# Performance work log

Measured on AMD Instinct MI355X. Metric: run time of the kernel, lower is better.

Reference implementation:

```python
import jax, jax.numpy as jnp
import numpy as np

NUM_CLASSES = 1000
FEAT = 192
HID = 256
TOTAL_NODES = 8192  # 16 images * 512 patches, kNN is global (no batch vector in source)


def _knn_idx(x, k):
    # squared euclidean distances, top-k smallest (self-loop included: d(i,i)=0)
    sq = jnp.sum(x * x, axis=-1)                       # [N]
    d = sq[:, None] + sq[None, :] - 2.0 * (x @ x.T)    # [N, N]
    _, idx = jax.lax.top_k(-d, k)                      # [N, k] neighbor indices per node
    return idx


def _sage_conv(x, idx, w_l, b_l, w_r):
    # PyG SAGEConv (mean aggr): lin_l(mean_j x_j) + lin_r(x_i); bias on lin_l
    agg = jnp.mean(x[idx], axis=1)                     # [N, C_in] mean over k neighbors
    return agg @ w_l + b_l + x @ w_r


def setup_inputs() -> dict:
    key = jax.random.key(0)
    ks = jax.random.split(key, 8)
    s = lambda fi, fo: (2.0 / (fi + fo)) ** 0.5
    return {
        "x": jax.random.normal(ks[0], (TOTAL_NODES, FEAT), dtype=jnp.float32),
        "w_l0": jax.random.normal(ks[1], (FEAT, HID), jnp.float32) * s(FEAT, HID),
        "b_l0": jnp.zeros((HID,), jnp.float32),
        "w_r0": jax.random.normal(ks[2], (FEAT, HID), jnp.float32) * s(FEAT, HID),
        "w_l1": jax.random.normal(ks[3], (HID, HID), jnp.float32) * s(HID, HID),
        "b_l1": jnp.zeros((HID,), jnp.float32),
        "w_r1": jax.random.normal(ks[4], (HID, HID), jnp.float32) * s(HID, HID),
        "w_l2": jax.random.normal(ks[5], (HID, NUM_CLASSES), jnp.float32) * s(HID, NUM_CLASSES),
        "b_l2": jnp.zeros((NUM_CLASSES,), jnp.float32),
        "w_r2": jax.random.normal(ks[6], (HID, NUM_CLASSES), jnp.float32) * s(HID, NUM_CLASSES),
        "k": 9,
        "batch_size": 16,
    }


def reference(x, w_l0, b_l0, w_r0, w_l1, b_l1, w_r1, w_l2, b_l2, w_r2, k, batch_size):
    idx = _knn_idx(x, k)  # graph built once from input features, reused by all layers
    h = jax.nn.relu(_sage_conv(x, idx, w_l0, b_l0, w_r0))
    h = jax.nn.relu(_sage_conv(h, idx, w_l1, b_l1, w_r1))
    h = jax.nn.relu(_sage_conv(h, idx, w_l2, b_l2, w_r2))
    # global_mean_pool with batch = arange(B).repeat_interleave(N/B): equal-size segments
    h = h.reshape(batch_size, -1, h.shape[-1]).mean(axis=1)  # [B, num_classes]
    return h
```

## Files before the change

kernel.cpp:

```cpp
#include <hip/hip_runtime.h>

#define NN   8192
#define FEAT 192
#define HID  256
#define NCLS 1000
#define KNN  9
#define NPP  512
#define NIMG 16
#define KD   192
#define KL0  384

typedef unsigned short ushort_t;
typedef unsigned int uint_t;
typedef __attribute__((ext_vector_type(8))) __bf16 bf16x8;
typedef __attribute__((ext_vector_type(4))) float f32x4;

#define ASYNC16(gptr, lptr)                                                  \
  __builtin_amdgcn_global_load_lds(                                          \
      (const __attribute__((address_space(1))) void*)(gptr),                 \
      (__attribute__((address_space(3))) void*)(lptr), 16, 0, 0)

__device__ __forceinline__ ushort_t f2bf_rne(float f) {
  unsigned u = __float_as_uint(f);
  u += 0x7FFF + ((u >> 16) & 1);
  return (ushort_t)(u >> 16);
}
__device__ __forceinline__ float bf2f(ushort_t u) {
  return __uint_as_float((unsigned)u << 16);
}

__device__ __forceinline__ uint_t packkey(float f, int col) {
  uint_t b = __float_as_uint(f);
  uint_t m = (uint_t)((int)b >> 31) | 0x80000000u;
  uint_t u = b ^ m;
  return (u & 0xFFFFE000u) | (uint_t)col;
}

__device__ __forceinline__ void bubble9(uint_t (&tk)[KNN], uint_t k) {
#pragma unroll
  for (int p = 0; p < KNN; ++p) {
    uint_t lo = min(tk[p], k);
    k = max(tk[p], k);
    tk[p] = lo;
  }
}

__global__ __launch_bounds__(256) void k_norms_split(
    const float* __restrict__ x, float* __restrict__ sq,
    ushort_t* __restrict__ xs) {
  int wid  = (blockIdx.x * 256 + threadIdx.x) >> 6;
  int lane = threadIdx.x & 63;
  if (wid >= NN) return;
  const float* row = x + (size_t)wid * FEAT;
  ushort_t* xr = xs + (size_t)wid * KD;
  float s = 0.f;
#pragma unroll
  for (int f0 = 0; f0 < FEAT; f0 += 64) {
    int f = f0 + lane;
    float v = row[f];
    s += v * v;
    xr[f] = f2bf_rne(v);
  }
#pragma unroll
  for (int off = 32; off > 0; off >>= 1) s += __shfl_down(s, off);
  if (lane == 0) sq[wid] = s;
}

__global__ __launch_bounds__(256, 4) void k_dist_topk(
    const ushort_t* __restrict__ xs, const float* __restrict__ sq,
    uint_t* __restrict__ cand) {
  __shared__ __align__(16) char smem[24576];
  ushort_t* As = (ushort_t*)smem;
  ushort_t* Bs = (ushort_t*)(smem + 8192);
  uint_t*   Ms = (uint_t*)(smem + 19456);

  const int t    = threadIdx.x;
  const int lane = t & 63;
  const int w    = t >> 6;
  const int l15  = lane & 15, lq = lane >> 4;
  const int rowStart = blockIdx.y * 128;
  const int colStart = blockIdx.x * 128;
  const int mrow = (w >> 1) * 64;
  const int ncol = (w & 1) * 64;

  const int m0 = w * 128 + lane;
  const int r0 = m0 >> 2, r1 = r0 + 16;
  const int g0 = m0 & 3;
  const int gs0 = g0 ^ (r0 & 3);
  const int gs1 = g0 ^ (r1 & 3);
  const ushort_t* gA0 = xs + (size_t)(rowStart + r0) * KD + gs0 * 8;
  const ushort_t* gA1 = xs + (size_t)(rowStart + r1) * KD + gs1 * 8;
  const ushort_t* gB0 = xs + (size_t)(colStart + r0) * KD + gs0 * 8;
  const ushort_t* gB1 = xs + (size_t)(colStart + r1) * KD + gs1 * 8;
  ushort_t* lA = As + w * 1024;
  ushort_t* lB = Bs + w * 1024;

  const int pg = (lq ^ (l15 & 3)) * 8;
  int aoff[4], boff[4];
#pragma unroll
  for (int ti = 0; ti < 4; ++ti) aoff[ti] = (mrow + ti * 16 + l15) * 32 + pg;
#pragma unroll
  for (int tj = 0; tj < 4; ++tj) boff[tj] = (ncol + tj * 16 + l15) * 32 + pg;

  f32x4 c00 = {}, c01 = {}, c02 = {}, c03 = {};
  f32x4 c10 = {}, c11 = {}, c12 = {}, c13 = {};
  f32x4 c20 = {}, c21 = {}, c22 = {}, c23 = {};
  f32x4 c30 = {}, c31 = {}, c32 = {}, c33 = {};

#pragma unroll 1
  for (int kt = 0; kt < 6; ++kt) {
    const int k0 = kt * 32;
    ASYNC16(gA0 + k0, lA);
    ASYNC16(gA1 + k0, lA + 512);
    ASYNC16(gB0 + k0, lB);
    ASYNC16(gB1 + k0, lB + 512);
    __syncthreads();
    bf16x8 a0 = *(const bf16x8*)(As + aoff[0]);
    bf16x8 a1 = *(const bf16x8*)(As + aoff[1]);
    bf16x8 a2 = *(const bf16x8*)(As + aoff[2]);
    bf16x8 a3 = *(const bf16x8*)(As + aoff[3]);
    bf16x8 b0 = *(const bf16x8*)(Bs + boff[0]);
    bf16x8 b1 = *(const bf16x8*)(Bs + boff[1]);
    bf16x8 b2 = *(const bf16x8*)(Bs + boff[2]);
    bf16x8 b3 = *(const bf16x8*)(Bs + boff[3]);
    c00 = __builtin_amdgcn_mfma_f32_16x16x32_bf16(a0, b0, c00, 0, 0, 0);
    c01 = __builtin_amdgcn_mfma_f32_16x16x32_bf16(a0, b1, c01, 0, 0, 0);
    c02 = __builtin_amdgcn_mfma_f32_16x16x32_bf16(a0, b2, c02, 0, 0, 0);
    c03 = __builtin_amdgcn_mfma_f32_16x16x32_bf16(a0, b3, c03, 0, 0, 0);
    c10 = __builtin_amdgcn_mfma_f32_16x16x32_bf16(a1, b0, c10, 0, 0, 0);
    c11 = __builtin_amdgcn_mfma_f32_16x16x32_bf16(a1, b1, c11, 0, 0, 0);
    c12 = __builtin_amdgcn_mfma_f32_16x16x32_bf16(a1, b2, c12, 0, 0, 0);
    c13 = __builtin_amdgcn_mfma_f32_16x16x32_bf16(a1, b3, c13, 0, 0, 0);
    c20 = __builtin_amdgcn_mfma_f32_16x16x32_bf16(a2, b0, c20, 0, 0, 0);
    c21 = __builtin_amdgcn_mfma_f32_16x16x32_bf16(a2, b1, c21, 0, 0, 0);
    c22 = __builtin_amdgcn_mfma_f32_16x16x32_bf16(a2, b2, c22, 0, 0, 0);
    c23 = __builtin_amdgcn_mfma_f32_16x16x32_bf16(a2, b3, c23, 0, 0, 0);
    c30 = __builtin_amdgcn_mfma_f32_16x16x32_bf16(a3, b0, c30, 0, 0, 0);
    c31 = __builtin_amdgcn_mfma_f32_16x16x32_bf16(a3, b1, c31, 0, 0, 0);
    c32 = __builtin_amdgcn_mfma_f32_16x16x32_bf16(a3, b2, c32, 0, 0, 0);
    c33 = __builtin_amdgcn_mfma_f32_16x16x32_bf16(a3, b3, c33, 0, 0, 0);
    __syncthreads();
  }

  uint_t tk[KNN];
#pragma unroll
  for (int n = 0; n < KNN; ++n) tk[n] = 0xFFFFFFFFu;

  uint_t* Ew = (uint_t*)smem + w * (64 * 19);

#define EPI_ROW(TI, CV)                                                      \
  do {                                                                       \
    f32x4 v_ = (CV);                                                         \
    Ew[((TI) * 16 + lq * 4 + 0) * 19 + l15] =                                \
        packkey(fmaf(-2.0f, v_.x, sqv), mycol);                              \
    Ew[((TI) * 16 + lq * 4 + 1) * 19 + l15] =                                \
        packkey(fmaf(-2.0f, v_.y, sqv), mycol);                              \
    Ew[((TI) * 16 + lq * 4 + 2) * 19 + l15] =                                \
        packkey(fmaf(-2.0f, v_.z, sqv), mycol);                              \
    Ew[((TI) * 16 + lq * 4 + 3) * 19 + l15] =                                \
        packkey(fmaf(-2.0f, v_.w, sqv), mycol);                              \
  } while (0)

#define EPI_TILE(TJ, C0, C1, C2, C3)                                         \
  do {                                                                       \
    int mycol = colStart + ncol + (TJ) * 16 + l15;                           \
    float sqv = sq[mycol];                                                   \
    EPI_ROW(0, C0); EPI_ROW(1, C1); EPI_ROW(2, C2); EPI_ROW(3, C3);          \
    _Pragma("unroll")                                                        \
    for (int c = 0; c < 16; ++c) bubble9(tk, Ew[lane * 19 + c]);             \
  } while (0)

  EPI_TILE(0, c00, c10, c20, c30);
  EPI_TILE(1, c01, c11, c21, c31);
  EPI_TILE(2, c02, c12, c22, c32);
  EPI_TILE(3, c03, c13, c23, c33);

  __syncthreads();
  if (w & 1) {
#pragma unroll
    for (int n = 0; n < KNN; ++n) Ms[(mrow + lane) * 10 + n] = tk[n];
  }
  __syncthreads();
  if (!(w & 1)) {
#pragma unroll
    for (int n = 0; n < KNN; ++n) bubble9(tk, Ms[(mrow + lane) * 10 + n]);
    size_t base = (((size_t)(rowStart + mrow + lane)) * 64 + blockIdx.x) * KNN;
#pragma unroll
    for (int n = 0; n < KNN; ++n) cand[base + n] = tk[n];
  }
}

__global__ __launch_bounds__(256) void k_reduce_gather(
    const uint_t* __restrict__ cand, const float* __restrict__ x,
    int* __restrict__ idx, ushort_t* __restrict__ Ab0) {
  int wid  = (blockIdx.x * 256 + threadIdx.x) >> 6;
  int lane = threadIdx.x & 63;
  if (wid >= NN) return;
  const uint_t* cv = cand + (size_t)wid * 576;
  uint_t tk[KNN];
#pragma unroll
  for (int n = 0; n < KNN; ++n) tk[n] = 0xFFFFFFFFu;
#pragma unroll
  for (int m = 0; m < KNN; ++m) bubble9(tk, cv[lane + 64 * m]);

  int nb[KNN];
  for (int r = 0; r < KNN; ++r) {
    uint_t bm = tk[0];
#pragma unroll
    for (int off = 32; off > 0; off >>= 1)
      bm = min(bm, (uint_t)__shfl_xor((unsigned int)bm, off));
    if (tk[0] == bm) {
#pragma unroll
      for (int p = 0; p < KNN - 1; ++p) tk[p] = tk[p + 1];
      tk[KNN - 1] = 0xFFFFFFFFu;
    }
    nb[r] = (int)(bm & 0x1FFFu);
    if (lane == 0) idx[wid * KNN + r] = nb[r];
  }

#pragma unroll
  for (int f0 = 0; f0 < FEAT; f0 += 64) {
    int f = f0 + lane;
    float s = 0.f;
#pragma unroll
    for (int n = 0; n < KNN; ++n) s += x[(size_t)nb[n] * FEAT + f];
    Ab0[(size_t)wid * KL0 + f]        = f2bf_rne(s * (1.0f / KNN));
    Ab0[(size_t)wid * KL0 + FEAT + f] = f2bf_rne(x[(size_t)wid * FEAT + f]);
  }
}

__global__ __launch_bounds__(256) void k_cast_w(
    const float* __restrict__ w_l0, const float* __restrict__ w_r0,
    const float* __restrict__ w_l1, const float* __restrict__ w_r1,
    const float* __restrict__ w_l2, const float* __restrict__ w_r2,
    ushort_t* __restrict__ WT0, ushort_t* __restrict__ WT1,
    ushort_t* __restrict__ WT2, float* __restrict__ out) {
  int i = blockIdx.x * 256 + threadIdx.x;
  if (i < NIMG * NCLS) out[i] = 0.f;
  if (i < 98304) {
    int n = i / 384, k = i - n * 384;
    float v = (k < 192) ? w_l0[k * 256 + n] : w_r0[(k - 192) * 256 + n];
    WT0[i] = f2bf_rne(v);
  } else if (i < 98304 + 131072) {
    int j = i - 98304;
    int n = j / 512, k = j - n * 512;
    float v = (k < 256) ? w_l1[k * 256 + n] : w_r1[(k - 256) * 256 + n];
    WT1[j] = f2bf_rne(v);
  } else {
    int j = i - (98304 + 131072);
    int n = j / 512, k = j - n * 512;
    float v = 0.f;
    if (n < NCLS)
      v = (k < 256) ? w_l2[k * NCLS + n] : w_r2[(k - 256) * NCLS + n];
    WT2[j] = f2bf_rne(v);
  }
}

__global__ __launch_bounds__(256) void k_gather_h(
    const ushort_t* __restrict__ hsrc, const int* __restrict__ idx,
    ushort_t* __restrict__ adst) {
  int wid  = (blockIdx.x * 256 + threadIdx.x) >> 6;
  int lane = threadIdx.x & 63;
  if (wid >= NN) return;
  int nb[KNN];
#pragma unroll
  for (int n = 0; n < KNN; ++n) nb[n] = idx[wid * KNN + n];
  const int c0 = lane * 4;
  float s0 = 0.f, s1 = 0.f, s2 = 0.f, s3 = 0.f;
#pragma unroll
  for (int n = 0; n < KNN; ++n) {
    ushort4 v = *(const ushort4*)(hsrc + (size_t)nb[n] * 512 + c0);
    s0 += bf2f(v.x); s1 += bf2f(v.y); s2 += bf2f(v.z); s3 += bf2f(v.w);
  }
  ushort4 o;
  o.x = f2bf_rne(s0 * (1.0f / KNN));
  o.y = f2bf_rne(s1 * (1.0f / KNN));
  o.z = f2bf_rne(s2 * (1.0f / KNN));
  o.w = f2bf_rne(s3 * (1.0f / KNN));
  *(ushort4*)(adst + (size_t)wid * 512 + c0) = o;
}

__global__ __launch_bounds__(256, 4) void k_sage64(
    const ushort_t* __restrict__ Ab, const ushort_t* __restrict__ WT,
    const float* __restrict__ bias, ushort_t* __restrict__ hdst, int KT) {
  __shared__ __align__(16) char smem[12288];
  ushort_t* As = (ushort_t*)smem;
  ushort_t* Bs = (ushort_t*)(smem + 8192);

  const int t    = threadIdx.x;
  const int lane = t & 63;
  const int w    = t >> 6;
  const int l15  = lane & 15, lq = lane >> 4;
  const int rowStart = blockIdx.y * 128;
  const int colStart = blockIdx.x * 64;
  const int mrow = (w >> 1) * 64;
  const int ncol = (w & 1) * 32;

  const int rA0 = t >> 2, rA1 = rA0 + 64;
  const int g   = t & 3;
  const int gsA0 = g ^ (rA0 & 3), gsA1 = g ^ (rA1 & 3);
  const ushort_t* gA0 = Ab + (size_t)(rowStart + rA0) * KT + gsA0 * 8;
  const ushort_t* gA1 = Ab + (size_t)(rowStart + rA1) * KT + gsA1 * 8;
  const ushort_t* gB0 = WT + (size_t)(colStart + rA0) * KT + gsA0 * 8;
  ushort_t* lA0 = As + w * 512;
  ushort_t* lA1 = As + 2048 + w * 512;
  ushort_t* lB0 = Bs + w * 512;

  const int pg = (lq ^ (l15 & 3)) * 8;
  int aoff[4], boff[2];
#pragma unroll
  for (int ti = 0; ti < 4; ++ti) aoff[ti] = (mrow + ti * 16 + l15) * 32 + pg;
#pragma unroll
  for (int tj = 0; tj < 2; ++tj) boff[tj] = (ncol + tj * 16 + l15) * 32 + pg;

  f32x4 c00 = {}, c01 = {};
  f32x4 c10 = {}, c11 = {};
  f32x4 c20 = {}, c21 = {};
  f32x4 c30 = {}, c31 = {};

  const int nkt = KT >> 5;
#pragma unroll 1
  for (int kt = 0; kt < nkt; ++kt) {
    const int k0 = kt * 32;
    ASYNC16(gA0 + k0, lA0);
    ASYNC16(gA1 + k0, lA1);
    ASYNC16(gB0 + k0, lB0);
    __syncthreads();
    bf16x8 a0 = *(const bf16x8*)(As + aoff[0]);
    bf16x8 a1 = *(const bf16x8*)(As + aoff[1]);
    bf16x8 a2 = *(const bf16x8*)(As + aoff[2]);
    bf16x8 a3 = *(const bf16x8*)(As + aoff[3]);
    bf16x8 b0 = *(const bf16x8*)(Bs + boff[0]);
    bf16x8 b1 = *(const bf16x8*)(Bs + boff[1]);
    c00 = __builtin_amdgcn_mfma_f32_16x16x32_bf16(a0, b0, c00, 0, 0, 0);
    c01 = __builtin_amdgcn_mfma_f32_16x16x32_bf16(a0, b1, c01, 0, 0, 0);
    c10 = __builtin_amdgcn_mfma_f32_16x16x32_bf16(a1, b0, c10, 0, 0, 0);
    c11 = __builtin_amdgcn_mfma_f32_16x16x32_bf16(a1, b1, c11, 0, 0, 0);
    c20 = __builtin_amdgcn_mfma_f32_16x16x32_bf16(a2, b0, c20, 0, 0, 0);
    c21 = __builtin_amdgcn_mfma_f32_16x16x32_bf16(a2, b1, c21, 0, 0, 0);
    c30 = __builtin_amdgcn_mfma_f32_16x16x32_bf16(a3, b0, c30, 0, 0, 0);
    c31 = __builtin_amdgcn_mfma_f32_16x16x32_bf16(a3, b1, c31, 0, 0, 0);
    __syncthreads();
  }

  const float bv0 = bias[colStart + ncol + l15];
  const float bv1 = bias[colStart + ncol + 16 + l15];

#define S64_STORE(TI, TJ, CV, BV)                                            \
  do {                                                                       \
    f32x4 v_ = (CV);                                                         \
    int col_ = colStart + ncol + (TJ) * 16 + l15;                            \
    size_t rb_ = (size_t)(rowStart + mrow + (TI) * 16 + lq * 4);             \
    hdst[(rb_ + 0) * 512 + col_] = f2bf_rne(fmaxf(v_.x + (BV), 0.f));        \
    hdst[(rb_ + 1) * 512 + col_] = f2bf_rne(fmaxf(v_.y + (BV), 0.f));        \
    hdst[(rb_ + 2) * 512 + col_] = f2bf_rne(fmaxf(v_.z + (BV), 0.f));        \
    hdst[(rb_ + 3) * 512 + col_] = f2bf_rne(fmaxf(v_.w + (BV), 0.f));        \
  } while (0)

  S64_STORE(0, 0, c00, bv0); S64_STORE(0, 1, c01, bv1);
  S64_STORE(1, 0, c10, bv0); S64_STORE(1, 1, c11, bv1);
  S64_STORE(2, 0, c20, bv0); S64_STORE(2, 1, c21, bv1);
  S64_STORE(3, 0, c30, bv0); S64_STORE(3, 1, c31, bv1);
}

__global__ __launch_bounds__(256, 2) void k_sage128_pool(
    const ushort_t* __restrict__ Ab, const ushort_t* __restrict__ WT,
    const float* __restrict__ bias, float* __restrict__ out) {
  __shared__ __align__(16) char smem[16384];
  ushort_t* As = (ushort_t*)smem;
  ushort_t* Bs = (ushort_t*)(smem + 8192);
  __shared__ float Ps[2][128];

  const int t    = threadIdx.x;
  const int lane = t & 63;
  const int w    = t >> 6;
  const int l15  = lane & 15, lq = lane >> 4;
  const int rowStart = blockIdx.y * 128;
  const int colStart = blockIdx.x * 128;
  const int mrow = (w >> 1) * 64;
  const int ncol = (w & 1) * 64;
  const int KT = 512;

  const int rA0 = t >> 2, rA1 = rA0 + 64;
  const int g   = t & 3;
  const int gsA0 = g ^ (rA0 & 3), gsA1 = g ^ (rA1 & 3);
  const ushort_t* gA0 = Ab + (size_t)(rowStart + rA0) * KT + gsA0 * 8;
  const ushort_t* gA1 = Ab + (size_t)(rowStart + rA1) * KT + gsA1 * 8;
  const ushort_t* gB0 = WT + (size_t)(colStart + rA0) * KT + gsA0 * 8;
  const ushort_t* gB1 = WT + (size_t)(colStart + rA1) * KT + gsA1 * 8;
  ushort_t* lA0 = As + w * 512;
  ushort_t* lA1 = As + 2048 + w * 512;
  ushort_t* lB0 = Bs + w * 512;
  ushort_t* lB1 = Bs + 2048 + w * 512;

  const int pg = (lq ^ (l15 & 3)) * 8;
  int aoff[4], boff[4];
#pragma unroll
  for (int ti = 0; ti < 4; ++ti) aoff[ti] = (mrow + ti * 16 + l15) * 32 + pg;
#pragma unroll
  for (int tj = 0; tj < 4; ++tj) boff[tj] = (ncol + tj * 16 + l15) * 32 + pg;

  f32x4 c00 = {}, c01 = {}, c02 = {}, c03 = {};
  f32x4 c10 = {}, c11 = {}, c12 = {}, c13 = {};
  f32x4 c20 = {}, c21 = {}, c22 = {}, c23 = {};
  f32x4 c30 = {}, c31 = {}, c32 = {}, c33 = {};

#pragma unroll 1
  for (int kt = 0; kt < 16; ++kt) {
    const int k0 = kt * 32;
    ASYNC16(gA0 + k0, lA0);
    ASYNC16(gA1 + k0, lA1);
    ASYNC16(gB0 + k0, lB0);
    ASYNC16(gB1 + k0, lB1);
    __syncthreads();
    bf16x8 a0 = *(const bf16x8*)(As + aoff[0]);
    bf16x8 a1 = *(const bf16x8*)(As + aoff[1]);
    bf16x8 a2 = *(const bf16x8*)(As + aoff[2]);
    bf16x8 a3 = *(const bf16x8*)(As + aoff[3]);
    bf16x8 b0 = *(const bf16x8*)(Bs + boff[0]);
    bf16x8 b1 = *(const bf16x8*)(Bs + boff[1]);
    bf16x8 b2 = *(const bf16x8*)(Bs + boff[2]);
    bf16x8 b3 = *(const bf16x8*)(Bs + boff[3]);
    c00 = __builtin_amdgcn_mfma_f32_16x16x32_bf16(a0, b0, c00, 0, 0, 0);
    c01 = __builtin_amdgcn_mfma_f32_16x16x32_bf16(a0, b1, c01, 0, 0, 0);
    c02 = __builtin_amdgcn_mfma_f32_16x16x32_bf16(a0, b2, c02, 0, 0, 0);
    c03 = __builtin_amdgcn_mfma_f32_16x16x32_bf16(a0, b3, c03, 0, 0, 0);
    c10 = __builtin_amdgcn_mfma_f32_16x16x32_bf16(a1, b0, c10, 0, 0, 0);
    c11 = __builtin_amdgcn_mfma_f32_16x16x32_bf16(a1, b1, c11, 0, 0, 0);
    c12 = __builtin_amdgcn_mfma_f32_16x16x32_bf16(a1, b2, c12, 0, 0, 0);
    c13 = __builtin_amdgcn_mfma_f32_16x16x32_bf16(a1, b3, c13, 0, 0, 0);
    c20 = __builtin_amdgcn_mfma_f32_16x16x32_bf16(a2, b0, c20, 0, 0, 0);
    c21 = __builtin_amdgcn_mfma_f32_16x16x32_bf16(a2, b1, c21, 0, 0, 0);
    c22 = __builtin_amdgcn_mfma_f32_16x16x32_bf16(a2, b2, c22, 0, 0, 0);
    c23 = __builtin_amdgcn_mfma_f32_16x16x32_bf16(a2, b3, c23, 0, 0, 0);
    c30 = __builtin_amdgcn_mfma_f32_16x16x32_bf16(a3, b0, c30, 0, 0, 0);
    c31 = __builtin_amdgcn_mfma_f32_16x16x32_bf16(a3, b1, c31, 0, 0, 0);
    c32 = __builtin_amdgcn_mfma_f32_16x16x32_bf16(a3, b2, c32, 0, 0, 0);
    c33 = __builtin_amdgcn_mfma_f32_16x16x32_bf16(a3, b3, c33, 0, 0, 0);
    __syncthreads();
  }

#define P_ACC(CV)                                                            \
  (fmaxf((CV).x + bv_, 0.f) + fmaxf((CV).y + bv_, 0.f) +                     \
   fmaxf((CV).z + bv_, 0.f) + fmaxf((CV).w + bv_, 0.f))

#define POOL_COL(TJ, C0, C1, C2, C3)                                         \
  do {                                                                       \
    int col_ = colStart + ncol + (TJ) * 16 + l15;                            \
    float bv_ = (col_ < NCLS) ? bias[col_] : 0.f;                            \
    float s_ = P_ACC(C0) + P_ACC(C1) + P_ACC(C2) + P_ACC(C3);                \
    s_ += __shfl_xor(s_, 16);                                                \
    s_ += __shfl_xor(s_, 32);                                                \
    if (lq == 0) Ps[w >> 1][ncol + (TJ) * 16 + l15] = s_;                    \
  } while (0)

  POOL_COL(0, c00, c10, c20, c30);
  POOL_COL(1, c01, c11, c21, c31);
  POOL_COL(2, c02, c12, c22, c32);
  POOL_COL(3, c03, c13, c23, c33);

  __syncthreads();
  if (t < 128) {
    int col = colStart + t;
    if (col < NCLS) {
      float s = Ps[0][t] + Ps[1][t];
      int img = rowStart / NPP;
      atomicAdd(out + (size_t)img * NCLS + col, s * (1.0f / NPP));
    }
  }
}

extern "C" void kernel_launch(void* const* d_in, const int* in_sizes, int n_in,
                              void* d_out, int out_size, void* d_ws,
                              size_t ws_size, hipStream_t stream) {
  const float* x    = (const float*)d_in[0];
  const float* w_l0 = (const float*)d_in[1];
  const float* b_l0 = (const float*)d_in[2];
  const float* w_r0 = (const float*)d_in[3];
  const float* w_l1 = (const float*)d_in[4];
  const float* b_l1 = (const float*)d_in[5];
  const float* w_r1 = (const float*)d_in[6];
  const float* w_l2 = (const float*)d_in[7];
  const float* b_l2 = (const float*)d_in[8];
  const float* w_r2 = (const float*)d_in[9];
  float* out = (float*)d_out;

  char* ws = (char*)d_ws;
  float*    sq   = (float*)(ws);
  int*      idx  = (int*)(ws + 32768);
  uint_t*   cand = (uint_t*)(ws + 327680);
  ushort_t* xs   = (ushort_t*)(ws + 19202048);
  ushort_t* Ab0  = (ushort_t*)(ws + 22347776);
  ushort_t* WT0  = (ushort_t*)(ws + 327680);
  ushort_t* WT1  = (ushort_t*)(ws + 524288);
  ushort_t* WT2  = (ushort_t*)(ws + 786432);
  ushort_t* Ab1  = (ushort_t*)(ws + 1835008);
  ushort_t* Ab2  = (ushort_t*)(ws + 10223616);

  k_norms_split<<<2048, 256, 0, stream>>>(x, sq, xs);
  k_dist_topk<<<dim3(64, 64), 256, 0, stream>>>(xs, sq, cand);
  k_reduce_gather<<<2048, 256, 0, stream>>>(cand, x, idx, Ab0);
  k_cast_w<<<2944, 256, 0, stream>>>(w_l0, w_r0, w_l1, w_r1, w_l2, w_r2,
                                     WT0, WT1, WT2, out);
  k_sage64<<<dim3(4, 64), 256, 0, stream>>>(Ab0, WT0, b_l0, Ab1 + 256, KL0);
  k_gather_h<<<2048, 256, 0, stream>>>(Ab1 + 256, idx, Ab1);
  k_sage64<<<dim3(4, 64), 256, 0, stream>>>(Ab1, WT1, b_l1, Ab2 + 256, 512);
  k_gather_h<<<2048, 256, 0, stream>>>(Ab2 + 256, idx, Ab2);
  k_sage128_pool<<<dim3(8, 64), 256, 0, stream>>>(Ab2, WT2, b_l2, out);
}
```

Measured before the change: 198.8 us.

## Fuse post-kNN layers into one persistent kernel with grid barriers

Merges the norm/split and weight-cast kernels into one prep launch. Replaces the reduce-gather, three SAGE GEMMs and two gather kernels with a single 512-block persistent kernel that separates stages with atomic-counter grid barriers. The aim is to remove per-launch gaps and tail effects across seven small dependent kernels. In exchange it relies on all 512 blocks being co-resident for the spin barrier to avoid deadlock, and each block now handles a fixed share of the work per stage.

```diff
diff --git a/kernel.cpp b/kernel.cpp
--- a/kernel.cpp
+++ b/kernel.cpp
@@ -9,6 +9,7 @@
 #define NIMG 16
 #define KD   192
 #define KL0  384
+#define NTB  512
 
 typedef unsigned short ushort_t;
 typedef unsigned int uint_t;
@@ -19,6 +20,8 @@
   __builtin_amdgcn_global_load_lds(                                          \
       (const __attribute__((address_space(1))) void*)(gptr),                 \
       (__attribute__((address_space(3))) void*)(lptr), 16, 0, 0)
+
+#define MFMA(a, b, c) __builtin_amdgcn_mfma_f32_16x16x32_bf16((a), (b), (c), 0, 0, 0)
 
 __device__ __forceinline__ ushort_t f2bf_rne(float f) {
   unsigned u = __float_as_uint(f);
@@ -45,197 +48,49 @@
   }
 }
 
-__global__ __launch_bounds__(256) void k_norms_split(
+__device__ __forceinline__ void gridbar(int* cnt, int target) {
+  __syncthreads();
+  if (threadIdx.x == 0) {
+    __threadfence();
+    atomicAdd(cnt, 1);
+    while (__hip_atomic_load(cnt, __ATOMIC_RELAXED,
+                             __HIP_MEMORY_SCOPE_AGENT) < target)
+      __builtin_amdgcn_s_sleep(4);
+    __threadfence();
+  }
+  __syncthreads();
+}
+
+__global__ __launch_bounds__(256) void k_prep(
     const float* __restrict__ x, float* __restrict__ sq,
-    ushort_t* __restrict__ xs) {
-  int wid  = (blockIdx.x * 256 + threadIdx.x) >> 6;
-  int lane = threadIdx.x & 63;
-  if (wid >= NN) return;
-  const float* row = x + (size_t)wid * FEAT;
-  ushort_t* xr = xs + (size_t)wid * KD;
-  float s = 0.f;
-#pragma unroll
-  for (int f0 = 0; f0 < FEAT; f0 += 64) {
-    int f = f0 + lane;
-    float v = row[f];
-    s += v * v;
-    xr[f] = f2bf_rne(v);
-  }
-#pragma unroll
-  for (int off = 32; off > 0; off >>= 1) s += __shfl_down(s, off);
-  if (lane == 0) sq[wid] = s;
-}
-
-__global__ __launch_bounds__(256, 4) void k_dist_topk(
-    const ushort_t* __restrict__ xs, const float* __restrict__ sq,
-    uint_t* __restrict__ cand) {
-  __shared__ __align__(16) char smem[24576];
-  ushort_t* As = (ushort_t*)smem;
-  ushort_t* Bs = (ushort_t*)(smem + 8192);
-  uint_t*   Ms = (uint_t*)(smem + 19456);
-
-  const int t    = threadIdx.x;
-  const int lane = t & 63;
-  const int w    = t >> 6;
-  const int l15  = lane & 15, lq = lane >> 4;
-  const int rowStart = blockIdx.y * 128;
-  const int colStart = blockIdx.x * 128;
-  const int mrow = (w >> 1) * 64;
-  const int ncol = (w & 1) * 64;
-
-  const int m0 = w * 128 + lane;
-  const int r0 = m0 >> 2, r1 = r0 + 16;
-  const int g0 = m0 & 3;
-  const int gs0 = g0 ^ (r0 & 3);
-  const int gs1 = g0 ^ (r1 & 3);
-  const ushort_t* gA0 = xs + (size_t)(rowStart + r0) * KD + gs0 * 8;
-  const ushort_t* gA1 = xs + (size_t)(rowStart + r1) * KD + gs1 * 8;
-  const ushort_t* gB0 = xs + (size_t)(colStart + r0) * KD + gs0 * 8;
-  const ushort_t* gB1 = xs + (size_t)(colStart + r1) * KD + gs1 * 8;
-  ushort_t* lA = As + w * 1024;
-  ushort_t* lB = Bs + w * 1024;
-
-  const int pg = (lq ^ (l15 & 3)) * 8;
-  int aoff[4], boff[4];
-#pragma unroll
-  for (int ti = 0; ti < 4; ++ti) aoff[ti] = (mrow + ti * 16 + l15) * 32 + pg;
-#pragma unroll
-  for (int tj = 0; tj < 4; ++tj) boff[tj] = (ncol + tj * 16 + l15) * 32 + pg;
-
-  f32x4 c00 = {}, c01 = {}, c02 = {}, c03 = {};
-  f32x4 c10 = {}, c11 = {}, c12 = {}, c13 = {};
-  f32x4 c20 = {}, c21 = {}, c22 = {}, c23 = {};
-  f32x4 c30 = {}, c31 = {}, c32 = {}, c33 = {};
-
-#pragma unroll 1
-  for (int kt = 0; kt < 6; ++kt) {
-    const int k0 = kt * 32;
-    ASYNC16(gA0 + k0, lA);
-    ASYNC16(gA1 + k0, lA + 512);
-    ASYNC16(gB0 + k0, lB);
-    ASYNC16(gB1 + k0, lB + 512);
-    __syncthreads();
-    bf16x8 a0 = *(const bf16x8*)(As + aoff[0]);
-    bf16x8 a1 = *(const bf16x8*)(As + aoff[1]);
-    bf16x8 a2 = *(const bf16x8*)(As + aoff[2]);
-    bf16x8 a3 = *(const bf16x8*)(As + aoff[3]);
-    bf16x8 b0 = *(const bf16x8*)(Bs + boff[0]);
-    bf16x8 b1 = *(const bf16x8*)(Bs + boff[1]);
-    bf16x8 b2 = *(const bf16x8*)(Bs + boff[2]);
-    bf16x8 b3 = *(const bf16x8*)(Bs + boff[3]);
-    c00 = __builtin_amdgcn_mfma_f32_16x16x32_bf16(a0, b0, c00, 0, 0, 0);
-    c01 = __builtin_amdgcn_mfma_f32_16x16x32_bf16(a0, b1, c01, 0, 0, 0);
-    c02 = __builtin_amdgcn_mfma_f32_16x16x32_bf16(a0, b2, c02, 0, 0, 0);
-    c03 = __builtin_amdgcn_mfma_f32_16x16x32_bf16(a0, b3, c03, 0, 0, 0);
-    c10 = __builtin_amdgcn_mfma_f32_16x16x32_bf16(a1, b0, c10, 0, 0, 0);
-    c11 = __builtin_amdgcn_mfma_f32_16x16x32_bf16(a1, b1, c11, 0, 0, 0);
-    c12 = __builtin_amdgcn_mfma_f32_16x16x32_bf16(a1, b2, c12, 0, 0, 0);
-    c13 = __builtin_amdgcn_mfma_f32_16x16x32_bf16(a1, b3, c13, 0, 0, 0);
-    c20 = __builtin_amdgcn_mfma_f32_16x16x32_bf16(a2, b0, c20, 0, 0, 0);
-    c21 = __builtin_amdgcn_mfma_f32_16x16x32_bf16(a2, b1, c21, 0, 0, 0);
-    c22 = __builtin_amdgcn_mfma_f32_16x16x32_bf16(a2, b2, c22, 0, 0, 0);
-    c23 = __builtin_amdgcn_mfma_f32_16x16x32_bf16(a2, b3, c23, 0, 0, 0);
-    c30 = __builtin_amdgcn_mfma_f32_16x16x32_bf16(a3, b0, c30, 0, 0, 0);
-    c31 = __builtin_amdgcn_mfma_f32_16x16x32_bf16(a3, b1, c31, 0, 0, 0);
-    c32 = __builtin_amdgcn_mfma_f32_16x16x32_bf16(a3, b2, c32, 0, 0, 0);
-    c33 = __builtin_amdgcn_mfma_f32_16x16x32_bf16(a3, b3, c33, 0, 0, 0);
-    __syncthreads();
-  }
-
-  uint_t tk[KNN];
-#pragma unroll
-  for (int n = 0; n < KNN; ++n) tk[n] = 0xFFFFFFFFu;
-
-  uint_t* Ew = (uint_t*)smem + w * (64 * 19);
-
-#define EPI_ROW(TI, CV)                                                      \
-  do {                                                                       \
-    f32x4 v_ = (CV);                                                         \
-    Ew[((TI) * 16 + lq * 4 + 0) * 19 + l15] =                                \
-        packkey(fmaf(-2.0f, v_.x, sqv), mycol);                              \
-    Ew[((TI) * 16 + lq * 4 + 1) * 19 + l15] =                                \
-        packkey(fmaf(-2.0f, v_.y, sqv), mycol);                              \
-    Ew[((TI) * 16 + lq * 4 + 2) * 19 + l15] =                                \
-        packkey(fmaf(-2.0f, v_.z, sqv), mycol);                              \
-    Ew[((TI) * 16 + lq * 4 + 3) * 19 + l15] =                                \
-        packkey(fmaf(-2.0f, v_.w, sqv), mycol);                              \
-  } while (0)
-
-#define EPI_TILE(TJ, C0, C1, C2, C3)                                         \
-  do {                                                                       \
-    int mycol = colStart + ncol + (TJ) * 16 + l15;                           \
-    float sqv = sq[mycol];                                                   \
-    EPI_ROW(0, C0); EPI_ROW(1, C1); EPI_ROW(2, C2); EPI_ROW(3, C3);          \
-    _Pragma("unroll")                                                        \
-    for (int c = 0; c < 16; ++c) bubble9(tk, Ew[lane * 19 + c]);             \
-  } while (0)
-
-  EPI_TILE(0, c00, c10, c20, c30);
-  EPI_TILE(1, c01, c11, c21, c31);
-  EPI_TILE(2, c02, c12, c22, c32);
-  EPI_TILE(3, c03, c13, c23, c33);
-
-  __syncthreads();
-  if (w & 1) {
-#pragma unroll
-    for (int n = 0; n < KNN; ++n) Ms[(mrow + lane) * 10 + n] = tk[n];
-  }
-  __syncthreads();
-  if (!(w & 1)) {
-#pragma unroll
-    for (int n = 0; n < KNN; ++n) bubble9(tk, Ms[(mrow + lane) * 10 + n]);
-    size_t base = (((size_t)(rowStart + mrow + lane)) * 64 + blockIdx.x) * KNN;
-#pragma unroll
-    for (int n = 0; n < KNN; ++n) cand[base + n] = tk[n];
-  }
-}
-
-__global__ __launch_bounds__(256) void k_reduce_gather(
-    const uint_t* __restrict__ cand, const float* __restrict__ x,
-    int* __restrict__ idx, ushort_t* __restrict__ Ab0) {
-  int wid  = (blockIdx.x * 256 + threadIdx.x) >> 6;
-  int lane = threadIdx.x & 63;
-  if (wid >= NN) return;
-  const uint_t* cv = cand + (size_t)wid * 576;
-  uint_t tk[KNN];
-#pragma unroll
-  for (int n = 0; n < KNN; ++n) tk[n] = 0xFFFFFFFFu;
-#pragma unroll
-  for (int m = 0; m < KNN; ++m) bubble9(tk, cv[lane + 64 * m]);
-
-  int nb[KNN];
-  for (int r = 0; r < KNN; ++r) {
-    uint_t bm = tk[0];
-#pragma unroll
-    for (int off = 32; off > 0; off >>= 1)
-      bm = min(bm, (uint_t)__shfl_xor((unsigned int)bm, off));
-    if (tk[0] == bm) {
-#pragma unroll
-      for (int p = 0; p < KNN - 1; ++p) tk[p] = tk[p + 1];
-      tk[KNN - 1] = 0xFFFFFFFFu;
-    }
-    nb[r] = (int)(bm & 0x1FFFu);
-    if (lane == 0) idx[wid * KNN + r] = nb[r];
-  }
-
-#pragma unroll
-  for (int f0 = 0; f0 < FEAT; f0 += 64) {
-    int f = f0 + lane;
-    float s = 0.f;
-#pragma unroll
-    for (int n = 0; n < KNN; ++n) s += x[(size_t)nb[n] * FEAT + f];
-    Ab0[(size_t)wid * KL0 + f]        = f2bf_rne(s * (1.0f / KNN));
-    Ab0[(size_t)wid * KL0 + FEAT + f] = f2bf_rne(x[(size_t)wid * FEAT + f]);
-  }
-}
-
-__global__ __launch_bounds__(256) void k_cast_w(
+    ushort_t* __restrict__ xs,
     const float* __restrict__ w_l0, const float* __restrict__ w_r0,
     const float* __restrict__ w_l1, const float* __restrict__ w_r1,
     const float* __restrict__ w_l2, const float* __restrict__ w_r2,
     ushort_t* __restrict__ WT0, ushort_t* __restrict__ WT1,
-    ushort_t* __restrict__ WT2, float* __restrict__ out) {
-  int i = blockIdx.x * 256 + threadIdx.x;
+    ushort_t* __restrict__ WT2, float* __restrict__ out,
+    int* __restrict__ cnt) {
+  const int blk = blockIdx.x, t = threadIdx.x;
+  if (blk < 2048) {
+    int wid  = (blk * 256 + t) >> 6;
+    int lane = t & 63;
+    const float* row = x + (size_t)wid * FEAT;
+    ushort_t* xr = xs + (size_t)wid * KD;
+    float s = 0.f;
+#pragma unroll
+    for (int f0 = 0; f0 < FEAT; f0 += 64) {
+      int f = f0 + lane;
+      float v = row[f];
+      s += v * v;
+      xr[f] = f2bf_rne(v);
+    }
+#pragma unroll
+    for (int off = 32; off > 0; off >>= 1) s += __shfl_down(s, off);
+    if (lane == 0) sq[wid] = s;
+    return;
+  }
+  int i = (blk - 2048) * 256 + t;
+  if (i == 0) *cnt = 0;
   if (i < NIMG * NCLS) out[i] = 0.f;
   if (i < 98304) {
     int n = i / 384, k = i - n * 384;
@@ -256,75 +111,54 @@
   }
 }
 
-__global__ __launch_bounds__(256) void k_gather_h(
-    const ushort_t* __restrict__ hsrc, const int* __restrict__ idx,
-    ushort_t* __restrict__ adst) {
-  int wid  = (blockIdx.x * 256 + threadIdx.x) >> 6;
-  int lane = threadIdx.x & 63;
-  if (wid >= NN) return;
-  int nb[KNN];
-#pragma unroll
-  for (int n = 0; n < KNN; ++n) nb[n] = idx[wid * KNN + n];
-  const int c0 = lane * 4;
-  float s0 = 0.f, s1 = 0.f, s2 = 0.f, s3 = 0.f;
-#pragma unroll
-  for (int n = 0; n < KNN; ++n) {
-    ushort4 v = *(const ushort4*)(hsrc + (size_t)nb[n] * 512 + c0);
-    s0 += bf2f(v.x); s1 += bf2f(v.y); s2 += bf2f(v.z); s3 += bf2f(v.w);
-  }
-  ushort4 o;
-  o.x = f2bf_rne(s0 * (1.0f / KNN));
-  o.y = f2bf_rne(s1 * (1.0f / KNN));
-  o.z = f2bf_rne(s2 * (1.0f / KNN));
-  o.w = f2bf_rne(s3 * (1.0f / KNN));
-  *(ushort4*)(adst + (size_t)wid * 512 + c0) = o;
-}
-
-__global__ __launch_bounds__(256, 4) void k_sage64(
-    const ushort_t* __restrict__ Ab, const ushort_t* __restrict__ WT,
-    const float* __restrict__ bias, ushort_t* __restrict__ hdst, int KT) {
-  __shared__ __align__(16) char smem[12288];
+__global__ __launch_bounds__(256, 4) void k_dist_topk(
+    const ushort_t* __restrict__ xs, const float* __restrict__ sq,
+    uint_t* __restrict__ cand) {
+  __shared__ __align__(16) char smem[24576];
   ushort_t* As = (ushort_t*)smem;
   ushort_t* Bs = (ushort_t*)(smem + 8192);
+  uint_t*   Ms = (uint_t*)(smem + 19456);
 
   const int t    = threadIdx.x;
   const int lane = t & 63;
   const int w    = t >> 6;
   const int l15  = lane & 15, lq = lane >> 4;
   const int rowStart = blockIdx.y * 128;
-  const int colStart = blockIdx.x * 64;
+  const int colStart = blockIdx.x * 128;
   const int mrow = (w >> 1) * 64;
-  const int ncol = (w & 1) * 32;
-
-  const int rA0 = t >> 2, rA1 = rA0 + 64;
-  const int g   = t & 3;
-  const int gsA0 = g ^ (rA0 & 3), gsA1 = g ^ (rA1 & 3);
-  const ushort_t* gA0 = Ab + (size_t)(rowStart + rA0) * KT + gsA0 * 8;
-  const ushort_t* gA1 = Ab + (size_t)(rowStart + rA1) * KT + gsA1 * 8;
-  const ushort_t* gB0 = WT + (size_t)(colStart + rA0) * KT + gsA0 * 8;
-  ushort_t* lA0 = As + w * 512;
-  ushort_t* lA1 = As + 2048 + w * 512;
-  ushort_t* lB0 = Bs + w * 512;
+  const int ncol = (w & 1) * 64;
+
+  const int m0 = w * 128 + lane;
+  const int r0 = m0 >> 2, r1 = r0 + 16;
+  const int g0 = m0 & 3;
+  const int gs0 = g0 ^ (r0 & 3);
+  const int gs1 = g0 ^ (r1 & 3);
+  const ushort_t* gA0 = xs + (size_t)(rowStart + r0) * KD + gs0 * 8;
+  const ushort_t* gA1 = xs + (size_t)(rowStart + r1) * KD + gs1 * 8;
+  const ushort_t* gB0 = xs + (size_t)(colStart + r0) * KD + gs0 * 8;
+  const ushort_t* gB1 = xs + (size_t)(colStart + r1) * KD + gs1 * 8;
+  ushort_t* lA = As + w * 1024;
+  ushort_t* lB = Bs + w * 1024;
 
   const int pg = (lq ^ (l15 & 3)) * 8;
-  int aoff[4], boff[2];
+  int aoff[4], boff[4];
 #pragma unroll
   for (int ti = 0; ti < 4; ++ti) aoff[ti] = (mrow + ti * 16 + l15) * 32 + pg;
 #pragma unroll
-  for (int tj = 0; tj < 2; ++tj) boff[tj] = (ncol + tj * 16 + l15) * 32 + pg;
-
-  f32x4 c00 = {}, c01 = {};
-  f32x4 c10 = {}, c11 = {};
-  f32x4 c20 = {}, c21 = {};
-  f32x4 c30 = {}, c31 = {};
-
-  const int nkt = KT >> 5;
+  for (int tj = 0; tj < 4; ++tj) boff[tj] = (ncol + tj * 16 + l15) * 32 + pg;
+
+  f32x4 c00 = {}, c01 = {}, c02 = {}, c03 = {};
+  f32x4 c10 = {}, c11 = {}, c12 = {}, c13 = {};
+  f32x4 c20 = {}, c21 = {}, c22 = {}, c23 = {};
+  f32x4 c30 = {}, c31 = {}, c32 = {}, c33 = {};
+
 #pragma unroll 1
-  for (int kt = 0; kt < nkt; ++kt) {
+  for (int kt = 0; kt < 6; ++kt) {
     const int k0 = kt * 32;
-    ASYNC16(gA0 + k0, lA0);
-    ASYNC16(gA1 + k0, lA1);
-    ASYNC16(gB0 + k0, lB0);
+    ASYNC16(gA0 + k0, lA);
+    ASYNC16(gA1 + k0, lA + 512);
+    ASYNC16(gB0 + k0, lB);
+    ASYNC16(gB1 + k0, lB + 512);
     __syncthreads();
     bf16x8 a0 = *(const bf16x8*)(As + aoff[0]);
     bf16x8 a1 = *(const bf16x8*)(As + aoff[1]);
@@ -332,21 +166,109 @@
     bf16x8 a3 = *(const bf16x8*)(As + aoff[3]);
     bf16x8 b0 = *(const bf16x8*)(Bs + boff[0]);
     bf16x8 b1 = *(const bf16x8*)(Bs + boff[1]);
-    c00 = __builtin_amdgcn_mfma_f32_16x16x32_bf16(a0, b0, c00, 0, 0, 0);
-    c01 = __builtin_amdgcn_mfma_f32_16x16x32_bf16(a0, b1, c01, 0, 0, 0);
-    c10 = __builtin_amdgcn_mfma_f32_16x16x32_bf16(a1, b0, c10, 0, 0, 0);
-    c11 = __builtin_amdgcn_mfma_f32_16x16x32_bf16(a1, b1, c11, 0, 0, 0);
-    c20 = __builtin_amdgcn_mfma_f32_16x16x32_bf16(a2, b0, c20, 0, 0, 0);
-    c21 = __builtin_amdgcn_mfma_f32_16x16x32_bf16(a2, b1, c21, 0, 0, 0);
-    c30 = __builtin_amdgcn_mfma_f32_16x16x32_bf16(a3, b0, c30, 0, 0, 0);
-    c31 = __builtin_amdgcn_mfma_f32_16x16x32_bf16(a3, b1, c31, 0, 0, 0);
+    bf16x8 b2 = *(const bf16x8*)(Bs + boff[2]);
+    bf16x8 b3 = *(const bf16x8*)(Bs + boff[3]);
+    c00 = MFMA(a0, b0, c00); c01 = MFMA(a0, b1, c01);
+    c02 = MFMA(a0, b2, c02); c03 = MFMA(a0, b3, c03);
+    c10 = MFMA(a1, b0, c10); c11 = MFMA(a1, b1, c11);
+    c12 = MFMA(a1, b2, c12); c13 = MFMA(a1, b3, c13);
+    c20 = MFMA(a2, b0, c20); c21 = MFMA(a2, b1, c21);
+    c22 = MFMA(a2, b2, c22); c23 = MFMA(a2, b3, c23);
+    c30 = MFMA(a3, b0, c30); c31 = MFMA(a3, b1, c31);
+    c32 = MFMA(a3, b2, c32); c33 = MFMA(a3, b3, c33);
+    __syncthreads();
+  }
+
+  uint_t tk[KNN];
+#pragma unroll
+  for (int n = 0; n < KNN; ++n) tk[n] = 0xFFFFFFFFu;
+
+  uint_t* Ew = (uint_t*)smem + w * (64 * 19);
+
+#define EPI_ROW(TI, CV)                                                      \
+  do {                                                                       \
+    f32x4 v_ = (CV);                                                         \
+    Ew[((TI) * 16 + lq * 4 + 0) * 19 + l15] =                                \
+        packkey(fmaf(-2.0f, v_.x, sqv), mycol);                              \
+    Ew[((TI) * 16 + lq * 4 + 1) * 19 + l15] =                                \
+        packkey(fmaf(-2.0f, v_.y, sqv), mycol);                              \
+    Ew[((TI) * 16 + lq * 4 + 2) * 19 + l15] =                                \
+        packkey(fmaf(-2.0f, v_.z, sqv), mycol);                              \
+    Ew[((TI) * 16 + lq * 4 + 3) * 19 + l15] =                                \
+        packkey(fmaf(-2.0f, v_.w, sqv), mycol);                              \
+  } while (0)
+
+#define EPI_TILE(TJ, C0, C1, C2, C3)                                         \
+  do {                                                                       \
+    int mycol = colStart + ncol + (TJ) * 16 + l15;                           \
+    float sqv = sq[mycol];                                                   \
+    EPI_ROW(0, C0); EPI_ROW(1, C1); EPI_ROW(2, C2); EPI_ROW(3, C3);          \
+    _Pragma("unroll")                                                        \
+    for (int c = 0; c < 16; ++c) bubble9(tk, Ew[lane * 19 + c]);             \
+  } while (0)
+
+  EPI_TILE(0, c00, c10, c20, c30);
+  EPI_TILE(1, c01, c11, c21, c31);
+  EPI_TILE(2, c02, c12, c22, c32);
+  EPI_TILE(3, c03, c13, c23, c33);
+
+  __syncthreads();
+  if (w & 1) {
+#pragma unroll
+    for (int n = 0; n < KNN; ++n) Ms[(mrow + lane) * 10 + n] = tk[n];
+  }
+  __syncthreads();
+  if (!(w & 1)) {
+#pragma unroll
+    for (int n = 0; n < KNN; ++n) bubble9(tk, Ms[(mrow + lane) * 10 + n]);
+    size_t base = (((size_t)(rowStart + mrow + lane)) * 64 + blockIdx.x) * KNN;
+#pragma unroll
+    for (int n = 0; n < KNN; ++n) cand[base + n] = tk[n];
+  }
+}
+
+__device__ __forceinline__ void sage64_dev(
+    const ushort_t* Ab, int KT, const ushort_t* WT, const float* bias,
+    ushort_t* hdst, int blk, char* smem) {
+  ushort_t* As = (ushort_t*)smem;
+  ushort_t* Bs = (ushort_t*)(smem + 4096);
+  const int t = threadIdx.x;
+  const int lane = t & 63, w = t >> 6;
+  const int l15 = lane & 15, lq = lane >> 4;
+  const int rowStart = (blk >> 2) * 64, colStart = (blk & 3) * 64;
+  const int mrow = (w >> 1) * 32, ncol = (w & 1) * 32;
+
+  const int rA = t >> 2, g = t & 3;
+  const int gs = g ^ (rA & 3);
+  const ushort_t* gA = Ab + (size_t)(rowStart + rA) * KT + gs * 8;
+  const ushort_t* gB = WT + (size_t)(colStart + rA) * KT + gs * 8;
+  ushort_t* lA = As + w * 512;
+  ushort_t* lB = Bs + w * 512;
+
+  const int pg = (lq ^ (l15 & 3)) * 8;
+  const int aoff0 = (mrow + l15) * 32 + pg, aoff1 = (mrow + 16 + l15) * 32 + pg;
+  const int boff0 = (ncol + l15) * 32 + pg, boff1 = (ncol + 16 + l15) * 32 + pg;
+
+  f32x4 c00 = {}, c01 = {}, c10 = {}, c11 = {};
+  const int nkt = KT >> 5;
+#pragma unroll 1
+  for (int kt = 0; kt < nkt; ++kt) {
+    const int k0 = kt * 32;
+    ASYNC16(gA + k0, lA);
+    ASYNC16(gB + k0, lB);
+    __syncthreads();
+    bf16x8 a0 = *(const bf16x8*)(As + aoff0);
+    bf16x8 a1 = *(const bf16x8*)(As + aoff1);
+    bf16x8 b0 = *(const bf16x8*)(Bs + boff0);
+    bf16x8 b1 = *(const bf16x8*)(Bs + boff1);
+    c00 = MFMA(a0, b0, c00); c01 = MFMA(a0, b1, c01);
+    c10 = MFMA(a1, b0, c10); c11 = MFMA(a1, b1, c11);
     __syncthreads();
   }
 
   const float bv0 = bias[colStart + ncol + l15];
   const float bv1 = bias[colStart + ncol + 16 + l15];
-
-#define S64_STORE(TI, TJ, CV, BV)                                            \
+#define S64_ST(TI, TJ, CV, BV)                                               \
   do {                                                                       \
     f32x4 v_ = (CV);                                                         \
     int col_ = colStart + ncol + (TJ) * 16 + l15;                            \
@@ -356,89 +278,158 @@
     hdst[(rb_ + 2) * 512 + col_] = f2bf_rne(fmaxf(v_.z + (BV), 0.f));        \
     hdst[(rb_ + 3) * 512 + col_] = f2bf_rne(fmaxf(v_.w + (BV), 0.f));        \
   } while (0)
-
-  S64_STORE(0, 0, c00, bv0); S64_STORE(0, 1, c01, bv1);
-  S64_STORE(1, 0, c10, bv0); S64_STORE(1, 1, c11, bv1);
-  S64_STORE(2, 0, c20, bv0); S64_STORE(2, 1, c21, bv1);
-  S64_STORE(3, 0, c30, bv0); S64_STORE(3, 1, c31, bv1);
-}
-
-__global__ __launch_bounds__(256, 2) void k_sage128_pool(
-    const ushort_t* __restrict__ Ab, const ushort_t* __restrict__ WT,
-    const float* __restrict__ bias, float* __restrict__ out) {
+  S64_ST(0, 0, c00, bv0); S64_ST(0, 1, c01, bv1);
+  S64_ST(1, 0, c10, bv0); S64_ST(1, 1, c11, bv1);
+}
+
+__device__ __forceinline__ void gather_h_dev(
+    const ushort_t* hsrc, const int* idx, ushort_t* adst, int blk) {
+  const int t = threadIdx.x;
+  const int lane = t & 63, w = t >> 6;
+  const int c0 = lane * 4;
+#pragma unroll 1
+  for (int it = 0; it < 4; ++it) {
+    int r = (blk * 4 + w) * 4 + it;
+    int nb[KNN];
+#pragma unroll
+    for (int n = 0; n < KNN; ++n) nb[n] = idx[r * KNN + n];
+    float s0 = 0.f, s1 = 0.f, s2 = 0.f, s3 = 0.f;
+#pragma unroll
+    for (int n = 0; n < KNN; ++n) {
+      ushort4 v = *(const ushort4*)(hsrc + (size_t)nb[n] * 512 + c0);
+      s0 += bf2f(v.x); s1 += bf2f(v.y); s2 += bf2f(v.z); s3 += bf2f(v.w);
+    }
+    ushort4 o;
+    o.x = f2bf_rne(s0 * (1.0f / KNN));
+    o.y = f2bf_rne(s1 * (1.0f / KNN));
+    o.z = f2bf_rne(s2 * (1.0f / KNN));
+    o.w = f2bf_rne(s3 * (1.0f / KNN));
+    *(ushort4*)(adst + (size_t)r * 512 + c0) = o;
+  }
+}
+
+__global__ __launch_bounds__(256) void k_tail(
+    const uint_t* __restrict__ cand, const float* __restrict__ x,
+    int* __restrict__ idx, ushort_t* __restrict__ Ab0,
+    const ushort_t* __restrict__ WT0, const float* __restrict__ b0,
+    ushort_t* __restrict__ Ab1,
+    const ushort_t* __restrict__ WT1, const float* __restrict__ b1,
+    ushort_t* __restrict__ Ab2,
+    const ushort_t* __restrict__ WT2, const float* __restrict__ b2,
+    float* __restrict__ out, int* __restrict__ cnt) {
   __shared__ __align__(16) char smem[16384];
-  ushort_t* As = (ushort_t*)smem;
-  ushort_t* Bs = (ushort_t*)(smem + 8192);
   __shared__ float Ps[2][128];
-
-  const int t    = threadIdx.x;
-  const int lane = t & 63;
-  const int w    = t >> 6;
-  const int l15  = lane & 15, lq = lane >> 4;
-  const int rowStart = blockIdx.y * 128;
-  const int colStart = blockIdx.x * 128;
-  const int mrow = (w >> 1) * 64;
-  const int ncol = (w & 1) * 64;
-  const int KT = 512;
-
-  const int rA0 = t >> 2, rA1 = rA0 + 64;
-  const int g   = t & 3;
-  const int gsA0 = g ^ (rA0 & 3), gsA1 = g ^ (rA1 & 3);
-  const ushort_t* gA0 = Ab + (size_t)(rowStart + rA0) * KT + gsA0 * 8;
-  const ushort_t* gA1 = Ab + (size_t)(rowStart + rA1) * KT + gsA1 * 8;
-  const ushort_t* gB0 = WT + (size_t)(colStart + rA0) * KT + gsA0 * 8;
-  const ushort_t* gB1 = WT + (size_t)(colStart + rA1) * KT + gsA1 * 8;
-  ushort_t* lA0 = As + w * 512;
-  ushort_t* lA1 = As + 2048 + w * 512;
-  ushort_t* lB0 = Bs + w * 512;
-  ushort_t* lB1 = Bs + 2048 + w * 512;
-
-  const int pg = (lq ^ (l15 & 3)) * 8;
-  int aoff[4], boff[4];
-#pragma unroll
-  for (int ti = 0; ti < 4; ++ti) aoff[ti] = (mrow + ti * 16 + l15) * 32 + pg;
-#pragma unroll
-  for (int tj = 0; tj < 4; ++tj) boff[tj] = (ncol + tj * 16 + l15) * 32 + pg;
-
-  f32x4 c00 = {}, c01 = {}, c02 = {}, c03 = {};
-  f32x4 c10 = {}, c11 = {}, c12 = {}, c13 = {};
-  f32x4 c20 = {}, c21 = {}, c22 = {}, c23 = {};
-  f32x4 c30 = {}, c31 = {}, c32 = {}, c33 = {};
+  const int blk = blockIdx.x;
+  const int t = threadIdx.x;
+  const int lane = t & 63, w = t >> 6;
 
 #pragma unroll 1
-  for (int kt = 0; kt < 16; ++kt) {
-    const int k0 = kt * 32;
-    ASYNC16(gA0 + k0, lA0);
-    ASYNC16(gA1 + k0, lA1);
-    ASYNC16(gB0 + k0, lB0);
-    ASYNC16(gB1 + k0, lB1);
-    __syncthreads();
-    bf16x8 a0 = *(const bf16x8*)(As + aoff[0]);
-    bf16x8 a1 = *(const bf16x8*)(As + aoff[1]);
-    bf16x8 a2 = *(const bf16x8*)(As + aoff[2]);
-    bf16x8 a3 = *(const bf16x8*)(As + aoff[3]);
-    bf16x8 b0 = *(const bf16x8*)(Bs + boff[0]);
-    bf16x8 b1 = *(const bf16x8*)(Bs + boff[1]);
-    bf16x8 b2 = *(const bf16x8*)(Bs + boff[2]);
-    bf16x8 b3 = *(const bf16x8*)(Bs + boff[3]);
-    c00 = __builtin_amdgcn_mfma_f32_16x16x32_bf16(a0, b0, c00, 0, 0, 0);
-    c01 = __builtin_amdgcn_mfma_f32_16x16x32_bf16(a0, b1, c01, 0, 0, 0);
-    c02 = __builtin_amdgcn_mfma_f32_16x16x32_bf16(a0, b2, c02, 0, 0, 0);
-    c03 = __builtin_amdgcn_mfma_f32_16x16x32_bf16(a0, b3, c03, 0, 0, 0);
-    c10 = __builtin_amdgcn_mfma_f32_16x16x32_bf16(a1, b0, c10, 0, 0, 0);
-    c11 = __builtin_amdgcn_mfma_f32_16x16x32_bf16(a1, b1, c11, 0, 0, 0);
-    c12 = __builtin_amdgcn_mfma_f32_16x16x32_bf16(a1, b2, c12, 0, 0, 0);
-    c13 = __builtin_amdgcn_mfma_f32_16x16x32_bf16(a1, b3, c13, 0, 0, 0);
-    c20 = __builtin_amdgcn_mfma_f32_16x16x32_bf16(a2, b0, c20, 0, 0, 0);
-    c21 = __builtin_amdgcn_mfma_f32_16x16x32_bf16(a2, b1, c21, 0, 0, 0);
-    c22 = __builtin_amdgcn_mfma_f32_16x16x32_bf16(a2, b2, c22, 0, 0, 0);
-    c23 = __builtin_amdgcn_mfma_f32_16x16x32_bf16(a2, b3, c23, 0, 0, 0);
-    c30 = __builtin_amdgcn_mfma_f32_16x16x32_bf16(a3, b0, c30, 0, 0, 0);
-    c31 = __builtin_amdgcn_mfma_f32_16x16x32_bf16(a3, b1, c31, 0, 0, 0);
-    c32 = __builtin_amdgcn_mfma_f32_16x16x32_bf16(a3, b2, c32, 0, 0, 0);
-    c33 = __builtin_amdgcn_mfma_f32_16x16x32_bf16(a3, b3, c33, 0, 0, 0);
-    __syncthreads();
-  }
+  for (int it = 0; it < 4; ++it) {
+    int r = (blk * 4 + w) * 4 + it;
+    const uint_t* cv = cand + (size_t)r * 576;
+    uint_t tk[KNN];
+#pragma unroll
+    for (int n = 0; n < KNN; ++n) tk[n] = 0xFFFFFFFFu;
+#pragma unroll
+    for (int m = 0; m < KNN; ++m) bubble9(tk, cv[lane + 64 * m]);
+    int nb[KNN];
+    for (int q = 0; q < KNN; ++q) {
+      uint_t bm = tk[0];
+#pragma unroll
+      for (int off = 32; off > 0; off >>= 1)
+        bm = min(bm, (uint_t)__shfl_xor((unsigned int)bm, off));
+      if (tk[0] == bm) {
+#pragma unroll
+        for (int p = 0; p < KNN - 1; ++p) tk[p] = tk[p + 1];
+        tk[KNN - 1] = 0xFFFFFFFFu;
+      }
+      nb[q] = (int)(bm & 0x1FFFu);
+      if (lane == 0) idx[r * KNN + q] = nb[q];
+    }
+#pragma unroll
+    for (int f0 = 0; f0 < FEAT; f0 += 64) {
+      int f = f0 + lane;
+      float s = 0.f;
+#pragma unroll
+      for (int n = 0; n < KNN; ++n) s += x[(size_t)nb[n] * FEAT + f];
+      Ab0[(size_t)r * KL0 + f]        = f2bf_rne(s * (1.0f / KNN));
+      Ab0[(size_t)r * KL0 + FEAT + f] = f2bf_rne(x[(size_t)r * FEAT + f]);
+    }
+  }
+  gridbar(cnt, 1 * NTB);
+
+  sage64_dev(Ab0, KL0, WT0, b0, Ab1 + 256, blk, smem);
+  gridbar(cnt, 2 * NTB);
+
+  gather_h_dev(Ab1 + 256, idx, Ab1, blk);
+  gridbar(cnt, 3 * NTB);
+
+  sage64_dev(Ab1, 512, WT1, b1, Ab2 + 256, blk, smem);
+  gridbar(cnt, 4 * NTB);
+
+  gather_h_dev(Ab2 + 256, idx, Ab2, blk);
+  gridbar(cnt, 5 * NTB);
+
+  {
+    ushort_t* As = (ushort_t*)smem;
+    ushort_t* Bs = (ushort_t*)(smem + 8192);
+    const int l15 = lane & 15, lq = lane >> 4;
+    const int rowStart = (blk >> 3) * 128;
+    const int colStart = (blk & 7) * 128;
+    const int mrow = (w >> 1) * 64;
+    const int ncol = (w & 1) * 64;
+    const int KT = 512;
+
+    const int rA0 = t >> 2, rA1 = rA0 + 64;
+    const int g = t & 3;
+    const int gsA0 = g ^ (rA0 & 3), gsA1 = g ^ (rA1 & 3);
+    const ushort_t* gA0 = Ab2 + (size_t)(rowStart + rA0) * KT + gsA0 * 8;
+    const ushort_t* gA1 = Ab2 + (size_t)(rowStart + rA1) * KT + gsA1 * 8;
+    const ushort_t* gB0 = WT2 + (size_t)(colStart + rA0) * KT + gsA0 * 8;
+    const ushort_t* gB1 = WT2 + (size_t)(colStart + rA1) * KT + gsA1 * 8;
+    ushort_t* lA0 = As + w * 512;
+    ushort_t* lA1 = As + 2048 + w * 512;
+    ushort_t* lB0 = Bs + w * 512;
+    ushort_t* lB1 = Bs + 2048 + w * 512;
+
+    const int pg = (lq ^ (l15 & 3)) * 8;
+    int aoff[4], boff[4];
+#pragma unroll
+    for (int ti = 0; ti < 4; ++ti) aoff[ti] = (mrow + ti * 16 + l15) * 32 + pg;
+#pragma unroll
+    for (int tj = 0; tj < 4; ++tj) boff[tj] = (ncol + tj * 16 + l15) * 32 + pg;
+
+    f32x4 c00 = {}, c01 = {}, c02 = {}, c03 = {};
+    f32x4 c10 = {}, c11 = {}, c12 = {}, c13 = {};
+    f32x4 c20 = {}, c21 = {}, c22 = {}, c23 = {};
+    f32x4 c30 = {}, c31 = {}, c32 = {}, c33 = {};
+
+#pragma unroll 1
+    for (int kt = 0; kt < 16; ++kt) {
+      const int k0 = kt * 32;
+      ASYNC16(gA0 + k0, lA0);
+      ASYNC16(gA1 + k0, lA1);
+      ASYNC16(gB0 + k0, lB0);
+      ASYNC16(gB1 + k0, lB1);
+      __syncthreads();
+      bf16x8 a0 = *(const bf16x8*)(As + aoff[0]);
+      bf16x8 a1 = *(const bf16x8*)(As + aoff[1]);
+      bf16x8 a2 = *(const bf16x8*)(As + aoff[2]);
+      bf16x8 a3 = *(const bf16x8*)(As + aoff[3]);
+      bf16x8 b0v = *(const bf16x8*)(Bs + boff[0]);
+      bf16x8 b1v = *(const bf16x8*)(Bs + boff[1]);
+      bf16x8 b2v = *(const bf16x8*)(Bs + boff[2]);
+      bf16x8 b3v = *(const bf16x8*)(Bs + boff[3]);
+      c00 = MFMA(a0, b0v, c00); c01 = MFMA(a0, b1v, c01);
+      c02 = MFMA(a0, b2v, c02); c03 = MFMA(a0, b3v, c03);
+      c10 = MFMA(a1, b0v, c10); c11 = MFMA(a1, b1v, c11);
+      c12 = MFMA(a1, b2v, c12); c13 = MFMA(a1, b3v, c13);
+      c20 = MFMA(a2, b0v, c20); c21 = MFMA(a2, b1v, c21);
+      c22 = MFMA(a2, b2v, c22); c23 = MFMA(a2, b3v, c23);
+      c30 = MFMA(a3, b0v, c30); c31 = MFMA(a3, b1v, c31);
+      c32 = MFMA(a3, b2v, c32); c33 = MFMA(a3, b3v, c33);
+      __syncthreads();
+    }
 
 #define P_ACC(CV)                                                            \
   (fmaxf((CV).x + bv_, 0.f) + fmaxf((CV).y + bv_, 0.f) +                     \
@@ -447,25 +438,26 @@
 #define POOL_COL(TJ, C0, C1, C2, C3)                                         \
   do {                                                                       \
     int col_ = colStart + ncol + (TJ) * 16 + l15;                            \
-    float bv_ = (col_ < NCLS) ? bias[col_] : 0.f;                            \
+    float bv_ = (col_ < NCLS) ? b2[col_] : 0.f;                              \
     float s_ = P_ACC(C0) + P_ACC(C1) + P_ACC(C2) + P_ACC(C3);                \
     s_ += __shfl_xor(s_, 16);                                                \
     s_ += __shfl_xor(s_, 32);                                                \
     if (lq == 0) Ps[w >> 1][ncol + (TJ) * 16 + l15] = s_;                    \
   } while (0)
 
-  POOL_COL(0, c00, c10, c20, c30);
-  POOL_COL(1, c01, c11, c21, c31);
-  POOL_COL(2, c02, c12, c22, c32);
-  POOL_COL(3, c03, c13, c23, c33);
-
-  __syncthreads();
-  if (t < 128) {
-    int col = colStart + t;
-    if (col < NCLS) {
-      float s = Ps[0][t] + Ps[1][t];
-      int img = rowStart / NPP;
-      atomicAdd(out + (size_t)img * NCLS + col, s * (1.0f / NPP));
+    POOL_COL(0, c00, c10, c20, c30);
+    POOL_COL(1, c01, c11, c21, c31);
+    POOL_COL(2, c02, c12, c22, c32);
+    POOL_COL(3, c03, c13, c23, c33);
+
+    __syncthreads();
+    if (t < 128) {
+      int col = colStart + t;
+      if (col < NCLS) {
+        float s = Ps[0][t] + Ps[1][t];
+        int img = rowStart / NPP;
+        atomicAdd(out + (size_t)img * NCLS + col, s * (1.0f / NPP));
+      }
     }
   }
 }
@@ -490,21 +482,17 @@
   int*      idx  = (int*)(ws + 32768);
   uint_t*   cand = (uint_t*)(ws + 327680);
   ushort_t* xs   = (ushort_t*)(ws + 19202048);
-  ushort_t* Ab0  = (ushort_t*)(ws + 22347776);
-  ushort_t* WT0  = (ushort_t*)(ws + 327680);
-  ushort_t* WT1  = (ushort_t*)(ws + 524288);
-  ushort_t* WT2  = (ushort_t*)(ws + 786432);
-  ushort_t* Ab1  = (ushort_t*)(ws + 1835008);
-  ushort_t* Ab2  = (ushort_t*)(ws + 10223616);
-
-  k_norms_split<<<2048, 256, 0, stream>>>(x, sq, xs);
+  ushort_t* Ab0  = (ushort_t*)(ws + 19202048);
+  ushort_t* Ab1  = (ushort_t*)(ws + 327680);
+  ushort_t* Ab2  = (ushort_t*)(ws + 8716288);
+  ushort_t* WT0  = (ushort_t*)(ws + 25493504);
+  ushort_t* WT1  = (ushort_t*)(ws + 25690112);
+  ushort_t* WT2  = (ushort_t*)(ws + 25952256);
+  int*      cnt  = (int*)(ws + 27000832);
+
+  k_prep<<<4992, 256, 0, stream>>>(x, sq, xs, w_l0, w_r0, w_l1, w_r1,
+                                   w_l2, w_r2, WT0, WT1, WT2, out, cnt);
   k_dist_topk<<<dim3(64, 64), 256, 0, stream>>>(xs, sq, cand);
-  k_reduce_gather<<<2048, 256, 0, stream>>>(cand, x, idx, Ab0);
-  k_cast_w<<<2944, 256, 0, stream>>>(w_l0, w_r0, w_l1, w_r1, w_l2, w_r2,
-                                     WT0, WT1, WT2, out);
-  k_sage64<<<dim3(4, 64), 256, 0, stream>>>(Ab0, WT0, b_l0, Ab1 + 256, KL0);
-  k_gather_h<<<2048, 256, 0, stream>>>(Ab1 + 256, idx, Ab1);
-  k_sage64<<<dim3(4, 64), 256, 0, stream>>>(Ab1, WT1, b_l1, Ab2 + 256, 512);
-  k_gather_h<<<2048, 256, 0, stream>>>(Ab2 + 256, idx, Ab2);
-  k_sage128_pool<<<dim3(8, 64), 256, 0, stream>>>(Ab2, WT2, b_l2, out);
-}
+  k_tail<<<NTB, 256, 0, stream>>>(cand, x, idx, Ab0, WT0, b_l0, Ab1,
+                                  WT1, b_l1, Ab2, WT2, b_l2, out, cnt);
+}
```

After: 445.3 us. +124.0%, slower.
